# Kernel tuning notes

Measured on AMD Instinct MI355X. Metric: run time of the kernel, lower is better.

Reference implementation:

```python
import jax, jax.numpy as jnp
import numpy as np

N_SPARSE = 2  # keep N of every M weights (2:4 structured sparsity)
M_SPARSE = 4


def compute_mask(w, n, m):
    # w: [out, in]; zero the (m - n) smallest-|w| entries in each group of m
    out_f, in_f = w.shape
    k = m - n
    wr = jnp.abs(w).reshape(out_f, in_f // m, m)
    # indices of the k smallest |w| per group (torch.topk largest=False)
    _, idx = jax.lax.top_k(-wr, k)                      # [out, in/m, k]
    pruned = jax.nn.one_hot(idx, m, dtype=w.dtype).sum(axis=-2)  # [out, in/m, m]
    mask = 1.0 - pruned
    return mask.reshape(out_f, in_f)


def setup_inputs() -> dict:
    key = jax.random.key(0)
    k1, k2, k3 = jax.random.split(key, 3)
    B, S, Din, Dout = 64, 197, 768, 3072
    x = jax.random.normal(k1, (B, S, Din), dtype=jnp.float32)
    weight = jax.random.normal(k2, (Dout, Din), dtype=jnp.float32)
    bias = jax.random.normal(k3, (Dout,), dtype=jnp.float32)
    return {"x": x, "weight": weight, "bias": bias}


def reference(x, weight, bias):
    # mask is a precomputed buffer in torch (not differentiated)
    mask = compute_mask(jax.lax.stop_gradient(weight), N_SPARSE, M_SPARSE)
    w = weight * mask
    # F.linear: x @ w.T + b
    return jnp.einsum('bsi,oi->bso', x, w) + bias
```

## Files before the change

kernel.cpp:

```cpp
#include <hip/hip_runtime.h>
#include <hip/hip_bf16.h>

#define M_DIM 12608
#define K_DIM 768
#define N_DIM 3072
#define M_PAD 12800
#define BM 256
#define BN 256
#define BK 32
#define NT (K_DIM / BK)
#define MBLK (M_PAD / BM)
#define NBLK_N (N_DIM / BN)
#define NWG (MBLK * NBLK_N)

typedef __attribute__((ext_vector_type(8))) short bf16x8;
typedef __attribute__((ext_vector_type(4))) float f32x4;

__device__ __forceinline__ void gload_lds16(const void* g, void* l) {
  __builtin_amdgcn_global_load_lds(
      (const __attribute__((address_space(1))) unsigned int*)g,
      (__attribute__((address_space(3))) unsigned int*)l,
      16, 0, 0);
}

#define GX 4800
#define GW 2304
__global__ void cvt_fused(const float* __restrict__ x, const float* __restrict__ w,
                          __hip_bfloat16* __restrict__ xb, __hip_bfloat16* __restrict__ wb) {
  if (blockIdx.x < GX) {
    size_t i = ((size_t)blockIdx.x * 256 + threadIdx.x) * 8;
    union { __hip_bfloat16 h[8]; uint4 u; } o;
    if (i < (size_t)M_DIM * K_DIM) {
      float4 a = *(const float4*)(x + i);
      float4 b = *(const float4*)(x + i + 4);
      o.h[0] = __float2bfloat16(a.x); o.h[1] = __float2bfloat16(a.y);
      o.h[2] = __float2bfloat16(a.z); o.h[3] = __float2bfloat16(a.w);
      o.h[4] = __float2bfloat16(b.x); o.h[5] = __float2bfloat16(b.y);
      o.h[6] = __float2bfloat16(b.z); o.h[7] = __float2bfloat16(b.w);
    } else {
      o.u = make_uint4(0, 0, 0, 0);
    }
    *(uint4*)(xb + i) = o.u;
  } else {
    size_t g = ((size_t)(blockIdx.x - GX) * 256 + threadIdx.x);
    float4 v = *(const float4*)(w + g * 4);
    float val[4] = {v.x, v.y, v.z, v.w};
    float a[4] = {fabsf(v.x), fabsf(v.y), fabsf(v.z), fabsf(v.w)};
    union { __hip_bfloat16 h[4]; uint2 u; } o;
#pragma unroll
    for (int i = 0; i < 4; ++i) {
      int rank = 0;
#pragma unroll
      for (int j = 0; j < 4; ++j)
        rank += (a[j] > a[i]) || (a[j] == a[i] && j > i);
      o.h[i] = __float2bfloat16(rank < 2 ? val[i] : 0.0f);
    }
    *(uint2*)(wb + g * 4) = o.u;
  }
}

__global__ __launch_bounds__(512, 2) void gemm_8p(
    const __hip_bfloat16* __restrict__ A,
    const __hip_bfloat16* __restrict__ B,
    const float* __restrict__ bias,
    float* __restrict__ C)
{
  extern __shared__ char smem[];

  const int tid  = threadIdx.x;
  const int lane = tid & 63;
  const int wave = tid >> 6;
  const int wm   = wave >> 2;
  const int wn   = wave & 3;

  const int wg  = blockIdx.x;
  const int swz = (wg & 7) * (NWG / 8) + (wg >> 3);
  const int tile_m = (swz / NBLK_N) * BM;
  const int tile_n = (swz % NBLK_N) * BN;

  const int r2 = lane >> 2;
  const int p  = lane & 3;
  const int fxor = (r2 & 3) ^ ((r2 >> 2) & 3);
  const int gsw  = p ^ fxor;
  const __hip_bfloat16* asrc[2];
  const __hip_bfloat16* bsrc[2];
#pragma unroll
  for (int u = 0; u < 2; ++u) {
    const int row = u * 128 + wave * 16 + r2;
    asrc[u] = A + (size_t)(tile_m + row) * K_DIM + gsw * 8;
    bsrc[u] = B + (size_t)(tile_n + row) * K_DIM + gsw * 8;
  }

  const int frow  = lane & 15;
  const int fslot = (lane >> 4) ^ (frow & 3) ^ ((frow >> 2) & 3);
  const int abase = (wm * 128 + frow) * 64 + fslot * 16;
  const int bbase = 16384 + (wn * 64 + frow) * 64 + fslot * 16;

  f32x4 acc[8][4] = {};

#pragma unroll
  for (int u = 0; u < 2; ++u)
    gload_lds16(asrc[u], smem + u * 8192 + wave * 1024);
#pragma unroll
  for (int u = 0; u < 2; ++u)
    gload_lds16(bsrc[u], smem + 16384 + u * 8192 + wave * 1024);
#pragma unroll
  for (int u = 0; u < 2; ++u)
    gload_lds16(asrc[u] + BK, smem + 32768 + u * 8192 + wave * 1024);
#pragma unroll
  for (int u = 0; u < 2; ++u)
    gload_lds16(bsrc[u] + BK, smem + 32768 + 16384 + u * 8192 + wave * 1024);
  asm volatile("s_waitcnt vmcnt(4)" ::: "memory");
  __builtin_amdgcn_s_barrier();

#pragma unroll
  for (int t = 0; t < NT; ++t) {
    const int q  = t & 3;
    const int qs = (t + 2) & 3;
    const char* bq = smem + q * 32768;

    bf16x8 af[4], bfv[4];
#pragma unroll
    for (int m = 0; m < 4; ++m)
      af[m] = *(const bf16x8*)(bq + abase + m * 1024);
#pragma unroll
    for (int n = 0; n < 4; ++n)
      bfv[n] = *(const bf16x8*)(bq + bbase + n * 1024);
    if (t + 2 < NT) {
#pragma unroll
      for (int u = 0; u < 2; ++u)
        gload_lds16(asrc[u] + (t + 2) * BK, smem + qs * 32768 + u * 8192 + wave * 1024);
    }
    __builtin_amdgcn_s_barrier();
    __builtin_amdgcn_s_setprio(1);
#pragma unroll
    for (int m = 0; m < 4; ++m)
#pragma unroll
      for (int n = 0; n < 4; ++n)
        acc[m][n] = __builtin_amdgcn_mfma_f32_16x16x32_bf16(af[m], bfv[n], acc[m][n], 0, 0, 0);
    __builtin_amdgcn_s_setprio(0);
    __builtin_amdgcn_s_barrier();

    bf16x8 af2[4];
#pragma unroll
    for (int m = 0; m < 4; ++m)
      af2[m] = *(const bf16x8*)(bq + abase + (4 + m) * 1024);
    if (t + 2 < NT) {
#pragma unroll
      for (int u = 0; u < 2; ++u)
        gload_lds16(bsrc[u] + (t + 2) * BK, smem + qs * 32768 + 16384 + u * 8192 + wave * 1024);
    }
    if (t < NT - 2)       { asm volatile("s_waitcnt vmcnt(4)" ::: "memory"); }
    else if (t == NT - 2) { asm volatile("s_waitcnt vmcnt(0)" ::: "memory"); }
    __builtin_amdgcn_s_barrier();
    __builtin_amdgcn_s_setprio(1);
#pragma unroll
    for (int m = 0; m < 4; ++m)
#pragma unroll
      for (int n = 0; n < 4; ++n)
        acc[4 + m][n] = __builtin_amdgcn_mfma_f32_16x16x32_bf16(af2[m], bfv[n], acc[4 + m][n], 0, 0, 0);
    __builtin_amdgcn_s_setprio(0);
    __builtin_amdgcn_s_barrier();
  }

  const int ccol = lane & 15;
  const int quad = lane >> 4;
  float bv[4];
#pragma unroll
  for (int n = 0; n < 4; ++n)
    bv[n] = bias[tile_n + wn * 64 + n * 16 + ccol];

  float* tr = (float*)smem + wave * 1088;
  const int erow = lane >> 2;
  const int es   = lane & 3;

#pragma unroll
  for (int m = 0; m < 8; ++m) {
#pragma unroll
    for (int n = 0; n < 4; ++n)
#pragma unroll
      for (int r = 0; r < 4; ++r)
        tr[(quad * 4 + r) * 68 + n * 16 + ccol] = acc[m][n][r] + bv[n];
    const int grow = tile_m + wm * 128 + m * 16 + erow;
    if (grow < M_DIM) {
      float* dst = C + (size_t)grow * N_DIM + tile_n + wn * 64;
#pragma unroll
      for (int u = 0; u < 4; ++u)
        *(f32x4*)(dst + u * 16 + es * 4) = *(const f32x4*)(tr + erow * 68 + u * 16 + es * 4);
    }
  }
}

extern "C" void kernel_launch(void* const* d_in, const int* in_sizes, int n_in,
                              void* d_out, int out_size, void* d_ws, size_t ws_size,
                              hipStream_t stream) {
  const float* x    = (const float*)d_in[0];
  const float* w    = (const float*)d_in[1];
  const float* bias = (const float*)d_in[2];
  float* out = (float*)d_out;

  __hip_bfloat16* xb = (__hip_bfloat16*)d_ws;
  __hip_bfloat16* wb = xb + (size_t)M_PAD * K_DIM;

  static bool attr_set = false;
  if (!attr_set) {
    hipFuncSetAttribute(reinterpret_cast<const void*>(gemm_8p),
                        hipFuncAttributeMaxDynamicSharedMemorySize, 131072);
    attr_set = true;
  }

  cvt_fused<<<GX + GW, 256, 0, stream>>>(x, w, xb, wb);
  gemm_8p<<<NWG, 512, 131072, stream>>>(xb, wb, bias, out);
}
```

Before: 248.3 us.

## Replace 256x256 4-stage GEMM with simpler 128x128 double-buffered kernel

Shrinks the GEMM tile from 256x256 with 8 waves and a 4-stage LDS pipeline to 128x128 with 4 waves and a 2-buffer static LDS scheme synchronised by __syncthreads each K step. It also drops the setprio and split-MFMA scheduling and writes outputs directly from registers as scalar stores instead of staging them through LDS for vectorised stores. The aim is more workgroups per CU and simpler synchronisation. In exchange it loses data reuse per tile, pipeline depth and coalesced 16-byte output stores.

```diff
diff --git a/kernel.cpp b/kernel.cpp
--- a/kernel.cpp
+++ b/kernel.cpp
@@ -5,13 +5,13 @@
 #define K_DIM 768
 #define N_DIM 3072
 #define M_PAD 12800
-#define BM 256
-#define BN 256
+#define BM 128
+#define BN 128
 #define BK 32
 #define NT (K_DIM / BK)
 #define MBLK (M_PAD / BM)
-#define NBLK_N (N_DIM / BN)
-#define NWG (MBLK * NBLK_N)
+#define NBLK (N_DIM / BN)
+#define NWG (MBLK * NBLK)
 
 typedef __attribute__((ext_vector_type(8))) short bf16x8;
 typedef __attribute__((ext_vector_type(4))) float f32x4;
@@ -59,66 +59,66 @@
   }
 }
 
-__global__ __launch_bounds__(512, 2) void gemm_8p(
+__global__ __launch_bounds__(256, 4) void gemm_bt(
     const __hip_bfloat16* __restrict__ A,
     const __hip_bfloat16* __restrict__ B,
     const float* __restrict__ bias,
     float* __restrict__ C)
 {
-  extern __shared__ char smem[];
+  __shared__ char smem[32768];
 
   const int tid  = threadIdx.x;
   const int lane = tid & 63;
   const int wave = tid >> 6;
-  const int wm   = wave >> 2;
-  const int wn   = wave & 3;
+  const int wm   = wave >> 1;
+  const int wn   = wave & 1;
 
   const int wg  = blockIdx.x;
   const int swz = (wg & 7) * (NWG / 8) + (wg >> 3);
-  const int tile_m = (swz / NBLK_N) * BM;
-  const int tile_n = (swz % NBLK_N) * BN;
+  const int tile_m = (swz / NBLK) * BM;
+  const int tile_n = (swz % NBLK) * BN;
 
   const int r2 = lane >> 2;
   const int p  = lane & 3;
-  const int fxor = (r2 & 3) ^ ((r2 >> 2) & 3);
-  const int gsw  = p ^ fxor;
+  const int gsw = p ^ (r2 & 3) ^ ((r2 >> 2) & 3);
   const __hip_bfloat16* asrc[2];
   const __hip_bfloat16* bsrc[2];
 #pragma unroll
   for (int u = 0; u < 2; ++u) {
-    const int row = u * 128 + wave * 16 + r2;
+    const int row = wave * 32 + u * 16 + r2;
     asrc[u] = A + (size_t)(tile_m + row) * K_DIM + gsw * 8;
     bsrc[u] = B + (size_t)(tile_n + row) * K_DIM + gsw * 8;
   }
 
   const int frow  = lane & 15;
   const int fslot = (lane >> 4) ^ (frow & 3) ^ ((frow >> 2) & 3);
-  const int abase = (wm * 128 + frow) * 64 + fslot * 16;
-  const int bbase = 16384 + (wn * 64 + frow) * 64 + fslot * 16;
+  const int abase = (wm * 64 + frow) * 64 + fslot * 16;
+  const int bbase = 8192 + (wn * 64 + frow) * 64 + fslot * 16;
 
-  f32x4 acc[8][4] = {};
+  f32x4 acc[4][4] = {};
 
 #pragma unroll
   for (int u = 0; u < 2; ++u)
-    gload_lds16(asrc[u], smem + u * 8192 + wave * 1024);
+    gload_lds16(asrc[u], smem + (wave * 2 + u) * 1024);
 #pragma unroll
   for (int u = 0; u < 2; ++u)
-    gload_lds16(bsrc[u], smem + 16384 + u * 8192 + wave * 1024);
+    gload_lds16(bsrc[u], smem + 8192 + (wave * 2 + u) * 1024);
+
+  for (int t = 0; t < NT; ++t) {
+    __syncthreads();
+
+    if (t + 1 < NT) {
+      char* nb = smem + ((t + 1) & 1) * 16384;
+      const int off = (t + 1) * BK;
 #pragma unroll
-  for (int u = 0; u < 2; ++u)
-    gload_lds16(asrc[u] + BK, smem + 32768 + u * 8192 + wave * 1024);
+      for (int u = 0; u < 2; ++u)
+        gload_lds16(asrc[u] + off, nb + (wave * 2 + u) * 1024);
 #pragma unroll
-  for (int u = 0; u < 2; ++u)
-    gload_lds16(bsrc[u] + BK, smem + 32768 + 16384 + u * 8192 + wave * 1024);
-  asm volatile("s_waitcnt vmcnt(4)" ::: "memory");
-  __builtin_amdgcn_s_barrier();
+      for (int u = 0; u < 2; ++u)
+        gload_lds16(bsrc[u] + off, nb + 8192 + (wave * 2 + u) * 1024);
+    }
 
-#pragma unroll
-  for (int t = 0; t < NT; ++t) {
-    const int q  = t & 3;
-    const int qs = (t + 2) & 3;
-    const char* bq = smem + q * 32768;
-
+    const char* bq = smem + (t & 1) * 16384;
     bf16x8 af[4], bfv[4];
 #pragma unroll
     for (int m = 0; m < 4; ++m)
@@ -126,41 +126,11 @@
 #pragma unroll
     for (int n = 0; n < 4; ++n)
       bfv[n] = *(const bf16x8*)(bq + bbase + n * 1024);
-    if (t + 2 < NT) {
-#pragma unroll
-      for (int u = 0; u < 2; ++u)
-        gload_lds16(asrc[u] + (t + 2) * BK, smem + qs * 32768 + u * 8192 + wave * 1024);
-    }
-    __builtin_amdgcn_s_barrier();
-    __builtin_amdgcn_s_setprio(1);
 #pragma unroll
     for (int m = 0; m < 4; ++m)
 #pragma unroll
       for (int n = 0; n < 4; ++n)
         acc[m][n] = __builtin_amdgcn_mfma_f32_16x16x32_bf16(af[m], bfv[n], acc[m][n], 0, 0, 0);
-    __builtin_amdgcn_s_setprio(0);
-    __builtin_amdgcn_s_barrier();
-
-    bf16x8 af2[4];
-#pragma unroll
-    for (int m = 0; m < 4; ++m)
-      af2[m] = *(const bf16x8*)(bq + abase + (4 + m) * 1024);
-    if (t + 2 < NT) {
-#pragma unroll
-      for (int u = 0; u < 2; ++u)
-        gload_lds16(bsrc[u] + (t + 2) * BK, smem + qs * 32768 + 16384 + u * 8192 + wave * 1024);
-    }
-    if (t < NT - 2)       { asm volatile("s_waitcnt vmcnt(4)" ::: "memory"); }
-    else if (t == NT - 2) { asm volatile("s_waitcnt vmcnt(0)" ::: "memory"); }
-    __builtin_amdgcn_s_barrier();
-    __builtin_amdgcn_s_setprio(1);
-#pragma unroll
-    for (int m = 0; m < 4; ++m)
-#pragma unroll
-      for (int n = 0; n < 4; ++n)
-        acc[4 + m][n] = __builtin_amdgcn_mfma_f32_16x16x32_bf16(af2[m], bfv[n], acc[4 + m][n], 0, 0, 0);
-    __builtin_amdgcn_s_setprio(0);
-    __builtin_amdgcn_s_barrier();
   }
 
   const int ccol = lane & 15;
@@ -170,23 +140,18 @@
   for (int n = 0; n < 4; ++n)
     bv[n] = bias[tile_n + wn * 64 + n * 16 + ccol];
 
-  float* tr = (float*)smem + wave * 1088;
-  const int erow = lane >> 2;
-  const int es   = lane & 3;
-
 #pragma unroll
-  for (int m = 0; m < 8; ++m) {
+  for (int m = 0; m < 4; ++m) {
+    const int rbase = tile_m + wm * 64 + m * 16 + quad * 4;
 #pragma unroll
-    for (int n = 0; n < 4; ++n)
+    for (int r = 0; r < 4; ++r) {
+      const int grow = rbase + r;
+      if (grow < M_DIM) {
+        float* crow = C + (size_t)grow * N_DIM + tile_n + wn * 64;
 #pragma unroll
-      for (int r = 0; r < 4; ++r)
-        tr[(quad * 4 + r) * 68 + n * 16 + ccol] = acc[m][n][r] + bv[n];
-    const int grow = tile_m + wm * 128 + m * 16 + erow;
-    if (grow < M_DIM) {
-      float* dst = C + (size_t)grow * N_DIM + tile_n + wn * 64;
-#pragma unroll
-      for (int u = 0; u < 4; ++u)
-        *(f32x4*)(dst + u * 16 + es * 4) = *(const f32x4*)(tr + erow * 68 + u * 16 + es * 4);
+        for (int n = 0; n < 4; ++n)
+          crow[n * 16 + ccol] = acc[m][n][r] + bv[n];
+      }
     }
   }
 }
@@ -202,13 +167,6 @@
   __hip_bfloat16* xb = (__hip_bfloat16*)d_ws;
   __hip_bfloat16* wb = xb + (size_t)M_PAD * K_DIM;
 
-  static bool attr_set = false;
-  if (!attr_set) {
-    hipFuncSetAttribute(reinterpret_cast<const void*>(gemm_8p),
-                        hipFuncAttributeMaxDynamicSharedMemorySize, 131072);
-    attr_set = true;
-  }
-
   cvt_fused<<<GX + GW, 256, 0, stream>>>(x, w, xb, wb);
-  gemm_8p<<<NWG, 512, 131072, stream>>>(xb, wb, bias, out);
+  gemm_bt<<<NWG, 256, 0, stream>>>(xb, wb, bias, out);
 }
```

After: 249.0 us. About the same (+0.3%).
